# Optimization experiments

Hardware: AMD Instinct MI355X
Metric: run time of the kernel (lower is better)

Reference implementation:

```python
import jax, jax.numpy as jnp
import numpy as np

V_PATCH_NUMS = (1, 2, 4, 6, 8, 10, 13, 16)
HW = 16
QUANT_RESI = 0.5
SHARE_K = 4
BETA = 1.0


def _pool_matrix(n_in, n_out):
    # adaptive average pooling as a [n_out, n_in] matrix (matches F.adaptive_avg_pool2d bins)
    P = np.zeros((n_out, n_in), np.float32)
    for i in range(n_out):
        s = (i * n_in) // n_out
        e = -((-(i + 1) * n_in) // n_out)  # ceil((i+1)*n_in/n_out)
        P[i, s:e] = 1.0 / (e - s)
    return jnp.asarray(P)


def _phi_index(si, SN):
    # PhiPartiallyShared.__getitem__(si/(SN-1)) with K=4 ticks
    K = SHARE_K
    ticks = np.linspace(1.0 / 3 / K, 1 - 1.0 / 3 / K, K) if K == 4 else np.linspace(1.0 / 2 / K, 1 - 1.0 / 2 / K, K)
    return int(np.argmin(np.abs(ticks - si / (SN - 1))))


def _phi(h, w, b):
    # Phi: h*(1-r) + conv3x3(h)*r, zero padding (nn.Conv2d default)
    y = jax.lax.conv_general_dilated(h, w, (1, 1), 'SAME',
                                     dimension_numbers=('NCHW', 'OIHW', 'NCHW'))
    y = y + b[None, :, None, None]
    return h * (1.0 - QUANT_RESI) + y * QUANT_RESI


def setup_inputs() -> dict:
    key = jax.random.key(0)
    k0, k1, k2 = jax.random.split(key, 3)
    B, C, V = 64, 32, 4096
    f = jax.random.normal(k0, (B, C, HW, HW), jnp.float32)
    embed = jax.random.normal(k1, (V, C), jnp.float32)  # EMAEmbedding.weight ~ randn
    phi_w = jax.random.normal(k2, (SHARE_K, C, C, 3, 3), jnp.float32) * (1.0 / np.sqrt(9.0 * C))
    phi_b = jnp.zeros((SHARE_K, C), jnp.float32)
    return {"f_BChw": f, "embed_weight": embed, "phi_w": phi_w, "phi_b": phi_b}


def reference(f_BChw, embed_weight, phi_w, phi_b):
    B, C, H, W = f_BChw.shape
    SN = len(V_PATCH_NUMS)
    f_ng = jax.lax.stop_gradient(f_BChw)
    f_hat = jnp.zeros_like(f_BChw)
    e_sq = jnp.sum(embed_weight * embed_weight, axis=1)  # [V]
    loss = jnp.float32(0.0)
    for si, pn in enumerate(V_PATCH_NUMS):
        rest = f_ng - jax.lax.stop_gradient(f_hat)  # residual to quantize (no grad through distance)
        if pn != H:
            P = _pool_matrix(H, pn)
            rest_d = jnp.einsum('oh,bchw,pw->bcop', P, rest, P)  # adaptive avg pool -> [B,C,pn,pn]
        else:
            rest_d = rest
        rest_NC = rest_d.transpose(0, 2, 3, 1).reshape(-1, C)  # [B*pn*pn, C]
        # squared euclidean cdist to codebook, argmin
        d = (jnp.sum(rest_NC * rest_NC, axis=1, keepdims=True)
             + e_sq[None, :]
             - 2.0 * (rest_NC @ embed_weight.T))  # [N, V]
        idx = jnp.argmin(d, axis=1)  # [B*pn*pn] int
        h = embed_weight[idx].reshape(B, pn, pn, C).transpose(0, 3, 1, 2)  # gather -> [B,C,pn,pn]
        if pn != H:
            h = jax.image.resize(h, (B, C, H, W), method='linear')  # bilinear, align_corners=False
        k = _phi_index(si, SN)
        h = _phi(h, phi_w[k], phi_b[k])
        f_hat = f_hat + h
        loss = loss + 0.25 * jnp.mean((jax.lax.stop_gradient(f_hat) - f_BChw) ** 2) \
                    + BETA * jnp.mean((f_hat - f_ng) ** 2)
    loss = loss / SN
    # straight-through estimator: grads flow to f_BChw as identity
    f_hat_st = jax.lax.stop_gradient(f_hat - f_BChw) + f_BChw
    return f_hat_st, loss
```

## Files before the change

kernel.cpp:

```cpp
#include <hip/hip_runtime.h>
#include <hip/hip_bf16.h>

#define BB 64
#define CC 32
#define HW2 256
#define VV 4096
#define NELEM (BB*CC*HW2)
#define PADW 18
#define PADA 324

#define OFF_F     0
#define OFF_FHAT  (OFF_F     + NELEM)
#define OFF_EMBT  (OFF_FHAT  + NELEM)
#define OFF_ESQ   (OFF_EMBT  + VV*CC)
#define OFF_PW    (OFF_ESQ   + VV)
#define OFF_PB    (OFF_PW    + 4*CC*CC*9)
#define OFF_REST  (OFF_PB    + 4*CC)
#define OFF_BESTA (OFF_REST  + 16384*CC)
#define OFF_BESTB (OFF_BESTA + 2*16384)
#define OFF_LOSS  (OFF_BESTB + 2*16384)
#define OFF_FLAG  (OFF_LOSS  + 1)

__device__ __forceinline__ int embt_idx(int v, int c) {
    return (v >> 6) * 2048 + c * 64 + (v & 63);
}

__global__ void k_probe(const void* __restrict__ fin, int* __restrict__ flag) {
    __shared__ int cnt[256];
    int t = threadIdx.x;
    const __hip_bfloat16* p = (const __hip_bfloat16*)fin;
    int local = 0;
    for (int i = t; i < 8192; i += 256) {
        float v = __bfloat162float(p[i]);
        if (!(fabsf(v) < 1e3f)) local++;
    }
    cnt[t] = local;
    __syncthreads();
    for (int s = 128; s > 0; s >>= 1) {
        if (t < s) cnt[t] += cnt[t + s];
        __syncthreads();
    }
    if (t == 0) *flag = (cnt[0] >= 64) ? 1 : 0;
}

__global__ void k_prep(const void* __restrict__ fin,
                       const void* __restrict__ ein,
                       const void* __restrict__ win,
                       const void* __restrict__ bin_,
                       const int* __restrict__ flag,
                       float* __restrict__ f, float* __restrict__ fhat,
                       float* __restrict__ embT, float* __restrict__ pw,
                       float* __restrict__ pb, float* __restrict__ loss) {
    bool isf32 = (*flag != 0);
    int i = blockIdx.x * 256 + threadIdx.x;
    if (i < NELEM) {
        f[i] = isf32 ? ((const float*)fin)[i]
                     : __bfloat162float(((const __hip_bfloat16*)fin)[i]);
        fhat[i] = 0.f;
    }
    if (i < VV*CC) {
        float ev = isf32 ? ((const float*)ein)[i]
                         : __bfloat162float(((const __hip_bfloat16*)ein)[i]);
        int v = i >> 5, c = i & 31;
        embT[embt_idx(v, c)] = ev;
    }
    if (i < 4*CC*CC*9)
        pw[i] = isf32 ? ((const float*)win)[i]
                      : __bfloat162float(((const __hip_bfloat16*)win)[i]);
    if (i < 4*CC)
        pb[i] = isf32 ? ((const float*)bin_)[i]
                      : __bfloat162float(((const __hip_bfloat16*)bin_)[i]);
    if (i == 0) *loss = 0.f;
}

__global__ void k_esq(const float* __restrict__ embT, float* __restrict__ esq) {
    int v = blockIdx.x * 256 + threadIdx.x;
    if (v >= VV) return;
    const float* p = embT + (v >> 6) * 2048 + (v & 63);
    float s = 0.f;
    #pragma unroll
    for (int c = 0; c < CC; ++c) { float e = p[c * 64]; s = fmaf(e, e, s); }
    esq[v] = s;
}

__global__ void k_pool0(const float* __restrict__ f, const float* __restrict__ fhat,
                        float* __restrict__ rest, unsigned long long* __restrict__ best) {
    int n = threadIdx.x;
    int c = blockIdx.y;
    if (n >= BB) return;
    if (c == 0) best[n] = 0xFFFFFFFFFFFFFFFFull;
    const float* fb = f + (n * CC + c) * HW2;
    const float* hb = fhat + (n * CC + c) * HW2;
    float s = 0.f;
    for (int h = 0; h < 16; ++h)
        for (int w = 0; w < 16; ++w)
            s += fb[h * 16 + w] - hb[h * 16 + w];
    rest[n * CC + c] = s * (1.f / 256.f);
}

__global__ __launch_bounds__(256, 4)
void k_argmin(const float* __restrict__ rest, const float* __restrict__ embT,
              const float* __restrict__ esq, unsigned long long* __restrict__ best,
              int Ntot, int cpw) {
    int tid  = threadIdx.x;
    int w    = tid >> 6, lane = tid & 63;
    int q0   = blockIdx.x * 512 + w * 128 + lane;
    int q1   = q0 + 64;
    int v0   = blockIdx.y * cpw;

    bool act0 = (q0 < Ntot), act1 = (q1 < Ntot);
    if (!act0 && !act1) return;
    int qa = act0 ? q0 : (Ntot - 1);
    int qb = act1 ? q1 : (Ntot - 1);

    float a0v[32], a1v[32];
    {
        const float4* ra = (const float4*)(rest + qa * CC);
        const float4* rb = (const float4*)(rest + qb * CC);
        #pragma unroll
        for (int c4 = 0; c4 < 8; ++c4) {
            float4 va = ra[c4], vb4 = rb[c4];
            a0v[c4*4+0] = va.x;  a0v[c4*4+1] = va.y;
            a0v[c4*4+2] = va.z;  a0v[c4*4+3] = va.w;
            a1v[c4*4+0] = vb4.x; a1v[c4*4+1] = vb4.y;
            a1v[c4*4+2] = vb4.z; a1v[c4*4+3] = vb4.w;
        }
    }

    float p0a = 0.f, p1a = 0.f, p0b = 0.f, p1b = 0.f;
    #pragma unroll
    for (int c = 0; c < 16; ++c)  p0a = fmaf(a0v[c], a0v[c], p0a);
    #pragma unroll
    for (int c = 16; c < 32; ++c) p1a = fmaf(a0v[c], a0v[c], p1a);
    #pragma unroll
    for (int c = 0; c < 16; ++c)  p0b = fmaf(a1v[c], a1v[c], p0b);
    #pragma unroll
    for (int c = 16; c < 32; ++c) p1b = fmaf(a1v[c], a1v[c], p1b);
    float xx0 = p0a + p1a;
    float xx1 = p0b + p1b;

    float bd0 = 3.4e38f, bd1 = 3.4e38f;
    int   bi0 = v0,      bi1 = v0;

    int ntiles = cpw >> 3;
    for (int t = 0; t < ntiles; ++t) {
        int vb = v0 + t * 8;
        int boff = __builtin_amdgcn_readfirstlane((vb >> 6) * 2048 + (vb & 63));
        int eoff = __builtin_amdgcn_readfirstlane(vb);
        const float* bt = embT + boff;
        const float* ep = esq + eoff;

        float acc0[8], acc1[8];
        #pragma unroll
        for (int j = 0; j < 8; ++j) { acc0[j] = 0.f; acc1[j] = 0.f; }

        #pragma unroll
        for (int k = 0; k < CC; ++k) {
            float a0 = a0v[k], a1 = a1v[k];
            #pragma unroll
            for (int j = 0; j < 8; ++j) {
                float bv = bt[k * 64 + j];
                acc0[j] = fmaf(a0, bv, acc0[j]);
                acc1[j] = fmaf(a1, bv, acc1[j]);
            }
        }

        #pragma unroll
        for (int j = 0; j < 8; ++j) {
            float es = ep[j];
            float d0 = fmaf(-2.f, acc0[j], xx0 + es);
            if (d0 < bd0) { bd0 = d0; bi0 = vb + j; }
            float d1 = fmaf(-2.f, acc1[j], xx1 + es);
            if (d1 < bd1) { bd1 = d1; bi1 = vb + j; }
        }
    }

    unsigned u0 = __float_as_uint(bd0);
    unsigned long long mono0 = (u0 & 0x80000000u)
        ? (unsigned long long)(~u0)
        : (unsigned long long)(u0 | 0x80000000u);
    unsigned long long pk0 = (mono0 << 32) | (unsigned long long)(unsigned)bi0;
    unsigned u1 = __float_as_uint(bd1);
    unsigned long long mono1 = (u1 & 0x80000000u)
        ? (unsigned long long)(~u1)
        : (unsigned long long)(u1 | 0x80000000u);
    unsigned long long pk1 = (mono1 << 32) | (unsigned long long)(unsigned)bi1;

    if (act0) atomicMin(best + q0, pk0);
    if (act1) atomicMin(best + q1, pk1);
}

__global__ __launch_bounds__(256)
void k_fuse(const float* __restrict__ embT,
            const unsigned long long* __restrict__ best,
            const float* __restrict__ pw, const float* __restrict__ pb,
            const float* __restrict__ f, float* __restrict__ fhat,
            float* __restrict__ loss,
            float* __restrict__ rest,
            unsigned long long* __restrict__ best_next,
            int pn, int k, int pn_next) {
    __shared__ float h_pad[CC * PADA];
    __shared__ float extra[CC * 169];
    __shared__ float red[4];
    int b = blockIdx.x, co8 = blockIdx.y, t = threadIdx.x;
    int nn = pn * pn;
    int y = t >> 4, x = t & 15;

    for (int i = t; i < CC * PADA; i += 256) h_pad[i] = 0.f;

    if (pn == 16) {
        __syncthreads();
        int id = (int)(unsigned)(best[b * HW2 + t] & 0xFFFFFFFFull);
        const float* er = embT + (id >> 6) * 2048 + (id & 63);
        int ctr = (y + 1) * PADW + (x + 1);
        #pragma unroll
        for (int c = 0; c < CC; ++c)
            h_pad[c * PADA + ctr] = er[c * 64];
    } else {
        float (*hs)[169] = (float(*)[169])extra;
        for (int cell = t; cell < nn; cell += 256) {
            int id = (int)(unsigned)(best[b * nn + cell] & 0xFFFFFFFFull);
            const float* er = embT + (id >> 6) * 2048 + (id & 63);
            #pragma unroll
            for (int c = 0; c < CC; ++c) hs[c][cell] = er[c * 64];
        }
        __syncthreads();
        float scale = (float)pn / 16.f;
        float sy = (y + 0.5f) * scale - 0.5f;
        sy = fminf(fmaxf(sy, 0.f), (float)(pn - 1));
        int y0 = (int)sy; int y1 = min(y0 + 1, pn - 1); float wy = sy - (float)y0;
        float sx = (x + 0.5f) * scale - 0.5f;
        sx = fminf(fmaxf(sx, 0.f), (float)(pn - 1));
        int x0 = (int)sx; int x1 = min(x0 + 1, pn - 1); float wx = sx - (float)x0;
        float wy0 = 1.f - wy, wx0 = 1.f - wx;
        int ctr = (y + 1) * PADW + (x + 1);
        #pragma unroll
        for (int c = 0; c < CC; ++c) {
            float v00 = hs[c][y0 * pn + x0], v01 = hs[c][y0 * pn + x1];
            float v10 = hs[c][y1 * pn + x0], v11 = hs[c][y1 * pn + x1];
            float a0 = wy0 * v00 + wy * v10;
            float a1 = wy0 * v01 + wy * v11;
            h_pad[c * PADA + ctr] = wx0 * a0 + wx * a1;
        }
    }
    __syncthreads();

    float acc[4];
    #pragma unroll
    for (int o = 0; o < 4; ++o) acc[o] = 0.f;
    const float* hbase = h_pad + y * PADW + x;
    const float* wpk = pw + (k * CC + co8 * 4) * (CC * 9);
    #pragma unroll
    for (int ci_ = 0; ci_ < CC; ++ci_) {
        float hv[9];
        #pragma unroll
        for (int dy = 0; dy < 3; ++dy)
            #pragma unroll
            for (int dx = 0; dx < 3; ++dx)
                hv[dy * 3 + dx] = hbase[ci_ * PADA + dy * PADW + dx];
        const float* wp = wpk + ci_ * 9;
        #pragma unroll
        for (int o = 0; o < 4; ++o) {
            const float* w9 = wp + o * (CC * 9);
            #pragma unroll
            for (int q = 0; q < 9; ++q) acc[o] = fmaf(hv[q], w9[q], acc[o]);
        }
    }

    float* diff = extra;
    float lsum = 0.f;
    int ctr = (y + 1) * PADW + (x + 1);
    #pragma unroll
    for (int o = 0; o < 4; ++o) {
        int co = co8 * 4 + o;
        float hval = h_pad[co * PADA + ctr];
        float outv = hval * 0.5f + (acc[o] + pb[k * CC + co]) * 0.5f;
        int pos = (b * CC + co) * HW2 + t;
        float fh = fhat[pos] + outv;
        fhat[pos] = fh;
        float dd = f[pos] - fh;
        diff[o * HW2 + t] = dd;
        lsum = fmaf(dd, dd, lsum);
    }
    #pragma unroll
    for (int off = 32; off > 0; off >>= 1) lsum += __shfl_down(lsum, off, 64);
    if ((t & 63) == 0) red[t >> 6] = lsum;
    __syncthreads();
    if (t == 0)
        atomicAdd(loss, red[0] + red[1] + red[2] + red[3]);

    if (pn_next > 0) {
        int nn2 = pn_next * pn_next;
        for (int q = t; q < nn2 * 4; q += 256) {
            int cell = q % nn2, o = q / nn2;
            int i = cell / pn_next, j = cell % pn_next;
            int s0 = (i * 16) / pn_next, e0 = ((i + 1) * 16 + pn_next - 1) / pn_next;
            int s1 = (j * 16) / pn_next, e1 = ((j + 1) * 16 + pn_next - 1) / pn_next;
            float inv = 1.f / (float)((e0 - s0) * (e1 - s1));
            float s = 0.f;
            for (int h = s0; h < e0; ++h)
                for (int w = s1; w < e1; ++w)
                    s += diff[o * HW2 + h * 16 + w];
            rest[(b * nn2 + cell) * CC + co8 * 4 + o] = s * inv;
        }
        if (co8 == 0)
            for (int q = t; q < nn2; q += 256)
                best_next[b * nn2 + q] = 0xFFFFFFFFFFFFFFFFull;
    }
}

__global__ void k_out(const float* __restrict__ fhat, const float* __restrict__ loss,
                      const int* __restrict__ flag, void* __restrict__ out) {
    bool isf32 = (*flag != 0);
    int i = blockIdx.x * 256 + threadIdx.x;
    if (i > NELEM) return;
    float v;
    if (i < NELEM) v = fhat[i];
    else           v = (*loss) * (1.25f / (float)NELEM / 8.f);
    if (isf32) ((float*)out)[i] = v;
    else       ((__hip_bfloat16*)out)[i] = __float2bfloat16(v);
}

extern "C" void kernel_launch(void* const* d_in, const int* in_sizes, int n_in,
                              void* d_out, int out_size, void* d_ws, size_t ws_size,
                              hipStream_t stream) {
    const void* fin  = d_in[0];
    const void* ein  = d_in[1];
    const void* win  = d_in[2];
    const void* bin_ = d_in[3];
    float* ws = (float*)d_ws;
    float* f    = ws + OFF_F;
    float* fhat = ws + OFF_FHAT;
    float* embT = ws + OFF_EMBT;
    float* esq  = ws + OFF_ESQ;
    float* pw   = ws + OFF_PW;
    float* pb   = ws + OFF_PB;
    float* rest = ws + OFF_REST;
    unsigned long long* bestA = (unsigned long long*)(ws + OFF_BESTA);
    unsigned long long* bestB = (unsigned long long*)(ws + OFF_BESTB);
    float* loss = ws + OFF_LOSS;
    int*   flag = (int*)(ws + OFF_FLAG);

    static const int PN[8] = {1, 2, 4, 6, 8, 10, 13, 16};
    static const int KK[8] = {0, 0, 1, 1, 2, 2, 3, 3};
    static const int SP[8] = {512, 512, 512, 256, 128, 128, 64, 32};

    k_probe<<<1, 256, 0, stream>>>(fin, flag);
    k_prep<<<(NELEM + 255) / 256, 256, 0, stream>>>(fin, ein, win, bin_, flag,
                                                    f, fhat, embT, pw, pb, loss);
    k_esq<<<(VV + 255) / 256, 256, 0, stream>>>(embT, esq);
    k_pool0<<<dim3(1, CC), 256, 0, stream>>>(f, fhat, rest, bestA);

    for (int si = 0; si < 8; ++si) {
        int pn = PN[si];
        int Ntot = BB * pn * pn;
        int Sp = SP[si];
        int cpw = VV / Sp;
        unsigned long long* bcur = (si & 1) ? bestB : bestA;
        unsigned long long* bnxt = (si & 1) ? bestA : bestB;
        int pn_next = (si < 7) ? PN[si + 1] : 0;
        int gx = (Ntot + 511) / 512;
        k_argmin<<<dim3(gx, Sp), 256, 0, stream>>>(rest, embT, esq, bcur, Ntot, cpw);
        k_fuse<<<dim3(BB, 8), 256, 0, stream>>>(embT, bcur, pw, pb, f, fhat, loss,
                                                rest, bnxt, pn, KK[si], pn_next);
    }
    k_out<<<(NELEM + 1 + 255) / 256, 256, 0, stream>>>(fhat, loss, flag, d_out);
}
```

Measured before the change: 447.1 us.

## Add shared-memory register-tiled argmin kernel for large scales

Adds a new distance/argmin kernel used for scales 4-7. It stages a 256-query by 128-code tile of queries and codebook entries in LDS, and each thread computes a 16x8 register block of dot products. The old kernel keeps serving the small scales. The goal is to cut global/L1 traffic and raise FMA reuse in the dominant N×V distance computation. In exchange the kernel uses more LDS and registers, so occupancy is lower, and the codebook split count per scale changes.

```diff
diff --git a/kernel.cpp b/kernel.cpp
--- a/kernel.cpp
+++ b/kernel.cpp
@@ -98,10 +98,133 @@
     rest[n * CC + c] = s * (1.f / 256.f);
 }
 
+__global__ __launch_bounds__(256, 2)
+void k_argmin_big(const float* __restrict__ rest, const float* __restrict__ embT,
+                  const float* __restrict__ esq, unsigned long long* __restrict__ best,
+                  int Ntot, int cpw) {
+    __shared__ float xT[CC * 256];
+    __shared__ float eT[CC * 128];
+    __shared__ float xxs[256];
+    int tid = threadIdx.x;
+    int tx = tid & 15, ty = tid >> 4;
+    int qblk = blockIdx.x * 256;
+    int v0 = blockIdx.y * cpw;
+    int t0 = v0 >> 6;
+
+    {
+        int qb = tid;
+        int qq = qblk + qb; if (qq > Ntot - 1) qq = Ntot - 1;
+        const float* xr = rest + qq * CC;
+        int col = ((qb >> 2) & 3) * 64 + (qb >> 4) * 4 + (qb & 3);
+        float p0 = 0.f, p1 = 0.f;
+        #pragma unroll
+        for (int c = 0; c < 16; ++c) {
+            float xv = xr[c];
+            xT[c * 256 + col] = xv;
+            p0 = fmaf(xv, xv, p0);
+        }
+        #pragma unroll
+        for (int c = 16; c < 32; ++c) {
+            float xv = xr[c];
+            xT[c * 256 + col] = xv;
+            p1 = fmaf(xv, xv, p1);
+        }
+        xxs[qb] = p0 + p1;
+    }
+    __syncthreads();
+
+    float xx[16];
+    #pragma unroll
+    for (int e = 0; e < 4; ++e) {
+        float4 t4 = *(const float4*)(xxs + ty * 16 + e * 4);
+        xx[e*4+0] = t4.x; xx[e*4+1] = t4.y; xx[e*4+2] = t4.z; xx[e*4+3] = t4.w;
+    }
+
+    float bd[16]; int bi[16];
+    #pragma unroll
+    for (int i = 0; i < 16; ++i) { bd[i] = 3.4e38f; bi[i] = v0; }
+
+    int ntiles = cpw >> 7;
+    for (int t = 0; t < ntiles; ++t) {
+        int vbase = v0 + t * 128;
+        const float* gt = embT + (size_t)(t0 + 2 * t) * 2048;
+        float4 s[4];
+        #pragma unroll
+        for (int i = 0; i < 4; ++i)
+            s[i] = *(const float4*)(gt + (tid + i * 256) * 4);
+        __syncthreads();
+        #pragma unroll
+        for (int i = 0; i < 4; ++i) {
+            int g = tid + i * 256;
+            int ss = g >> 9, r = g & 511;
+            int c = r >> 4, j4 = r & 15;
+            int p = (j4 & 1) * 16 + ss * 8 + (j4 >> 1);
+            *(float4*)(eT + c * 128 + p * 4) = s[i];
+        }
+        __syncthreads();
+
+        float acc[16][8];
+        #pragma unroll
+        for (int i = 0; i < 16; ++i)
+            #pragma unroll
+            for (int j = 0; j < 8; ++j) acc[i][j] = 0.f;
+
+        #pragma unroll 2
+        for (int k = 0; k < CC; ++k) {
+            const float* xk = xT + k * 256;
+            const float* ek = eT + k * 128;
+            float4 A0 = *(const float4*)(xk + ty * 4);
+            float4 A1 = *(const float4*)(xk + 64 + ty * 4);
+            float4 A2 = *(const float4*)(xk + 128 + ty * 4);
+            float4 A3 = *(const float4*)(xk + 192 + ty * 4);
+            float4 B0 = *(const float4*)(ek + tx * 4);
+            float4 B1 = *(const float4*)(ek + 64 + tx * 4);
+            float a[16] = {A0.x,A0.y,A0.z,A0.w, A1.x,A1.y,A1.z,A1.w,
+                           A2.x,A2.y,A2.z,A2.w, A3.x,A3.y,A3.z,A3.w};
+            float b[8]  = {B0.x,B0.y,B0.z,B0.w, B1.x,B1.y,B1.z,B1.w};
+            #pragma unroll
+            for (int i = 0; i < 16; ++i)
+                #pragma unroll
+                for (int j = 0; j < 8; ++j)
+                    acc[i][j] = fmaf(a[i], b[j], acc[i][j]);
+        }
+
+        float4 e0 = *(const float4*)(esq + vbase + tx * 8);
+        float4 e1 = *(const float4*)(esq + vbase + tx * 8 + 4);
+        float es[8] = {e0.x,e0.y,e0.z,e0.w, e1.x,e1.y,e1.z,e1.w};
+        #pragma unroll
+        for (int i = 0; i < 16; ++i) {
+            float base = xx[i];
+            #pragma unroll
+            for (int j = 0; j < 8; ++j) {
+                float dist = fmaf(-2.f, acc[i][j], base + es[j]);
+                if (dist < bd[i]) { bd[i] = dist; bi[i] = vbase + tx * 8 + j; }
+            }
+        }
+    }
+
+    #pragma unroll
+    for (int i = 0; i < 16; ++i) {
+        unsigned u = __float_as_uint(bd[i]);
+        unsigned long long mono = (u & 0x80000000u)
+            ? (unsigned long long)(~u)
+            : (unsigned long long)(u | 0x80000000u);
+        unsigned long long pk = (mono << 32) | (unsigned long long)(unsigned)bi[i];
+        #pragma unroll
+        for (int m = 1; m <= 8; m <<= 1) {
+            unsigned long long o = __shfl_xor(pk, m, 64);
+            if (o < pk) pk = o;
+        }
+        int q = qblk + ty * 16 + i;
+        if (tx == 0 && q < Ntot)
+            atomicMin(best + q, pk);
+    }
+}
+
 __global__ __launch_bounds__(256, 4)
-void k_argmin(const float* __restrict__ rest, const float* __restrict__ embT,
-              const float* __restrict__ esq, unsigned long long* __restrict__ best,
-              int Ntot, int cpw) {
+void k_argmin_small(const float* __restrict__ rest, const float* __restrict__ embT,
+                    const float* __restrict__ esq, unsigned long long* __restrict__ best,
+                    int Ntot, int cpw) {
     int tid  = threadIdx.x;
     int w    = tid >> 6, lane = tid & 63;
     int q0   = blockIdx.x * 512 + w * 128 + lane;
@@ -343,7 +466,8 @@
 
     static const int PN[8] = {1, 2, 4, 6, 8, 10, 13, 16};
     static const int KK[8] = {0, 0, 1, 1, 2, 2, 3, 3};
-    static const int SP[8] = {512, 512, 512, 256, 128, 128, 64, 32};
+    static const int SPs[4] = {512, 512, 512, 256};
+    static const int SPb[4] = {32, 32, 16, 16};
 
     k_probe<<<1, 256, 0, stream>>>(fin, flag);
     k_prep<<<(NELEM + 255) / 256, 256, 0, stream>>>(fin, ein, win, bin_, flag,
@@ -354,13 +478,22 @@
     for (int si = 0; si < 8; ++si) {
         int pn = PN[si];
         int Ntot = BB * pn * pn;
-        int Sp = SP[si];
-        int cpw = VV / Sp;
         unsigned long long* bcur = (si & 1) ? bestB : bestA;
         unsigned long long* bnxt = (si & 1) ? bestA : bestB;
         int pn_next = (si < 7) ? PN[si + 1] : 0;
-        int gx = (Ntot + 511) / 512;
-        k_argmin<<<dim3(gx, Sp), 256, 0, stream>>>(rest, embT, esq, bcur, Ntot, cpw);
+        if (si < 4) {
+            int Sp = SPs[si];
+            int cpw = VV / Sp;
+            int gx = (Ntot + 511) / 512;
+            k_argmin_small<<<dim3(gx, Sp), 256, 0, stream>>>(rest, embT, esq, bcur,
+                                                             Ntot, cpw);
+        } else {
+            int Sp = SPb[si - 4];
+            int cpw = VV / Sp;
+            int gx = (Ntot + 255) / 256;
+            k_argmin_big<<<dim3(gx, Sp), 256, 0, stream>>>(rest, embT, esq, bcur,
+                                                           Ntot, cpw);
+        }
         k_fuse<<<dim3(BB, 8), 256, 0, stream>>>(embT, bcur, pw, pb, f, fhat, loss,
                                                 rest, bnxt, pn, KK[si], pn_next);
     }
```

Result: slower. 471.6 us (+5.5%).
